# Performance work log

Hardware: AMD Instinct MI355X
Metric: run time of the kernel (lower is better)

## Reference

```python
import jax, jax.numpy as jnp
import numpy as np

DIM = 64
N = 10000
E = 40000


def setup_inputs() -> dict:
    key = jax.random.key(0)
    ks = jax.random.split(key, 16)
    def rn(k, shape, s):
        return jax.random.normal(k, shape, dtype=jnp.float32) * s
    inp = {}
    inp["x"] = jax.random.normal(ks[0], (N, 3), dtype=jnp.float32)
    inp["edge_attr"] = jax.random.uniform(ks[1], (E, 7), dtype=jnp.float32)
    inp["edge_index"] = jax.random.randint(ks[2], (2, E), 0, N)
    inp["batch"] = jnp.zeros((N,), dtype=jnp.int32)
    # lin0: Linear(3, dim)
    inp["lin0_w"] = rn(ks[3], (DIM, 3), 0.3)
    inp["lin0_b"] = jnp.zeros((DIM,), jnp.float32)
    # edge MLP: Linear(7, dim) -> ReLU -> Linear(dim, dim*dim)
    inp["em1_w"] = rn(ks[4], (DIM, 7), 0.3)
    inp["em1_b"] = jnp.zeros((DIM,), jnp.float32)
    inp["em2_w"] = rn(ks[5], (DIM * DIM, DIM), 0.05)
    inp["em2_b"] = jnp.zeros((DIM * DIM,), jnp.float32)
    # NNConv root weight [in, out] and bias
    inp["root_w"] = rn(ks[6], (DIM, DIM), 0.1)
    inp["conv_b"] = jnp.zeros((DIM,), jnp.float32)
    # GRU(dim, dim), gate order r, z, n
    inp["gru_wih"] = rn(ks[7], (3 * DIM, DIM), 0.1)
    inp["gru_whh"] = rn(ks[8], (3 * DIM, DIM), 0.1)
    inp["gru_bih"] = jnp.zeros((3 * DIM,), jnp.float32)
    inp["gru_bhh"] = jnp.zeros((3 * DIM,), jnp.float32)
    # Set2Set LSTM(2*dim, dim), gate order i, f, g, o
    inp["lstm_wih"] = rn(ks[9], (4 * DIM, 2 * DIM), 0.1)
    inp["lstm_whh"] = rn(ks[10], (4 * DIM, DIM), 0.1)
    inp["lstm_bih"] = jnp.zeros((4 * DIM,), jnp.float32)
    inp["lstm_bhh"] = jnp.zeros((4 * DIM,), jnp.float32)
    inp["lin1_w"] = rn(ks[11], (DIM, 2 * DIM), 0.1)
    inp["lin1_b"] = jnp.zeros((DIM,), jnp.float32)
    inp["lin3_w"] = rn(ks[12], (1, DIM), 0.1)
    inp["lin3_b"] = jnp.zeros((1,), jnp.float32)
    return inp


def _forward(x, edge_attr, lin0_w, lin0_b, em1_w, em1_b, em2_w, em2_b,
             root_w, conv_b, gru_wih, gru_whh, gru_bih, gru_bhh,
             lstm_wih, lstm_whh, lstm_bih, lstm_bhh,
             lin1_w, lin1_b, lin3_w, lin3_b, edge_index, batch):
    n = x.shape[0]
    dim = lin0_w.shape[0]
    src, dst = edge_index[0], edge_index[1]

    out = jax.nn.relu(x @ lin0_w.T + lin0_b)  # [N, dim]
    h = out                                   # GRU hidden state

    # Edge-conditioned weights depend only on edge_attr -> compute once.
    we = jax.nn.relu(edge_attr @ em1_w.T + em1_b) @ em2_w.T + em2_b
    we = we.reshape(-1, dim, dim)             # [E, dim, dim]

    deg = jax.ops.segment_sum(jnp.ones_like(src, dtype=x.dtype), dst, num_segments=n)
    inv_deg = jnp.where(deg > 0, 1.0 / jnp.maximum(deg, 1.0), 0.0)[:, None]

    for _ in range(6):
        # NNConv: per-edge matmul, scatter-mean, plus root transform
        msg = jnp.einsum('ei,eio->eo', out[src], we)            # [E, dim]
        agg = jax.ops.segment_sum(msg, dst, num_segments=n) * inv_deg
        m = jax.nn.relu(out @ root_w + agg + conv_b)            # [N, dim]
        # single-step GRU over nodes (seq_len=1, batch=N)
        gi = m @ gru_wih.T + gru_bih
        gh = h @ gru_whh.T + gru_bhh
        ir, iz, inew = jnp.split(gi, 3, axis=-1)
        hr, hz, hnew = jnp.split(gh, 3, axis=-1)
        r = jax.nn.sigmoid(ir + hr)
        z = jax.nn.sigmoid(iz + hz)
        ncand = jnp.tanh(inew + r * hnew)
        h = (1.0 - z) * ncand + z * h
        out = h

    # Set2Set pooling; single graph (batch is all zeros, pool.view(1,-1))
    q_star = jnp.zeros((1, 2 * dim), x.dtype)
    hl = jnp.zeros((1, dim), x.dtype)
    cl = jnp.zeros((1, dim), x.dtype)
    for _ in range(6):
        g = q_star @ lstm_wih.T + lstm_bih + hl @ lstm_whh.T + lstm_bhh
        gi_, gf_, gg_, go_ = jnp.split(g, 4, axis=-1)
        cl = jax.nn.sigmoid(gf_) * cl + jax.nn.sigmoid(gi_) * jnp.tanh(gg_)
        hl = jax.nn.sigmoid(go_) * jnp.tanh(cl)
        q = hl                                                  # [1, dim]
        e = jnp.einsum('nd,d->n', out, q[0])                    # attention logits
        a = jax.nn.softmax(e)                                   # softmax over the single graph
        r = jnp.einsum('n,nd->d', a, out)[None, :]              # readout [1, dim]
        q_star = jnp.concatenate([q, r], axis=-1)               # [1, 2*dim]

    pool = q_star.reshape(1, -1)
    hid = jax.nn.relu(pool @ lin1_w.T + lin1_b)
    return hid @ lin3_w.T + lin3_b                              # [1, 1]


def reference(x, edge_attr, edge_index, batch, lin0_w, lin0_b, em1_w, em1_b,
              em2_w, em2_b, root_w, conv_b, gru_wih, gru_whh, gru_bih, gru_bhh,
              lstm_wih, lstm_whh, lstm_bih, lstm_bhh, lin1_w, lin1_b, lin3_w, lin3_b):
    return _forward(x, edge_attr, lin0_w, lin0_b, em1_w, em1_b, em2_w, em2_b,
                    root_w, conv_b, gru_wih, gru_whh, gru_bih, gru_bhh,
                    lstm_wih, lstm_whh, lstm_bih, lstm_bhh,
                    lin1_w, lin1_b, lin3_w, lin3_b, edge_index, batch)
```

## Files before the change

### kernel.cpp

```cpp
#include <hip/hip_runtime.h>
#include <math.h>

#define NNODES 10000
#define NEDGES 40000
#define DIM 64
#define WS 200
#define EB 128
#define H1S 68
#define OTS 72
#define BSS 72

typedef short bf16x8 __attribute__((ext_vector_type(8)));
typedef float floatx4 __attribute__((ext_vector_type(4)));

__device__ __forceinline__ float sigmoidf_(float x) { return 1.0f / (1.0f + expf(-x)); }

__device__ __forceinline__ unsigned short f2bf(float x) {
    unsigned int u = __float_as_uint(x);
    u += 0x7fffu + ((u >> 16) & 1u);
    return (unsigned short)(u >> 16);
}
__device__ __forceinline__ float bf2f(unsigned short h) {
    return __uint_as_float(((unsigned int)h) << 16);
}
__device__ __forceinline__ unsigned int cvtpk(float lo, float hi) {
    unsigned int r;
    asm("v_cvt_pk_bf16_f32 %0, %1, %2" : "=v"(r) : "v"(lo), "v"(hi));
    return r;
}
__device__ __forceinline__ void write_split(unsigned short* __restrict__ p, int d, float v) {
    unsigned short hi = f2bf(v);
    unsigned short lo = f2bf(v - bf2f(hi));
    p[d] = hi;
    p[64 + d] = hi;
    p[128 + d] = lo;
}

__global__ __launch_bounds__(256) void k_prep(const float* __restrict__ x,
                                              const float* __restrict__ lin0_w,
                                              const float* __restrict__ lin0_b,
                                              float* __restrict__ out,
                                              unsigned short* __restrict__ Abf,
                                              const float* __restrict__ em2_w,
                                              const float* __restrict__ em2_b,
                                              unsigned short* __restrict__ Bek,
                                              const float* __restrict__ root_w,
                                              const float* __restrict__ gwih,
                                              const float* __restrict__ gwhh,
                                              unsigned short* __restrict__ Wcat,
                                              const float* __restrict__ lwih,
                                              const float* __restrict__ lwhh,
                                              float* __restrict__ wcT,
                                              float* __restrict__ wrT,
                                              const int* __restrict__ ei,
                                              int* __restrict__ counts,
                                              float* __restrict__ deg) {
    const int b = blockIdx.x;
    const int tid = threadIdx.x;
    if (b < 2500) {
        int idx = b * 256 + tid;
        if (idx >= NNODES * 64) return;
        int n = idx >> 6, d = idx & 63;
        float a = lin0_b[d];
        a += x[n * 3 + 0] * lin0_w[d * 3 + 0];
        a += x[n * 3 + 1] * lin0_w[d * 3 + 1];
        a += x[n * 3 + 2] * lin0_w[d * 3 + 2];
        float v = fmaxf(a, 0.0f);
        out[idx] = v;
        write_split(Abf + (size_t)n * 192, d, v);
    } else if (b < 3540) {
        int idx = (b - 2500) * 256 + tid;
        if (idx >= 4160 * 64) return;
        int r = idx >> 6, k = idx & 63;
        float v = (r < 4096) ? em2_w[(size_t)r * 64 + k] : em2_b[k * 64 + (r - 4096)];
        Bek[idx] = f2bf(v);
    } else if (b < 3652) {
        int idx = (b - 3540) * 256 + tid;
        if (idx >= 448 * 64) return;
        int r = idx >> 6, i = idx & 63;
        float v;
        if (r < 64) v = root_w[i * 64 + r];
        else if (r < 256) v = gwih[(r - 64) * 64 + i];
        else v = gwhh[(r - 256) * 64 + i];
        unsigned short hi = f2bf(v);
        unsigned short lo = f2bf(v - bf2f(hi));
        unsigned short* row = Wcat + (size_t)r * 192;
        row[i] = hi;
        row[64 + i] = lo;
        row[128 + i] = hi;
    } else if (b < 3780) {
        int idx = (b - 3652) * 256 + tid;
        if (idx < 64 * 256) {
            int k = idx >> 8, t = idx & 255;
            wcT[idx] = lwih[t * 128 + k] + lwhh[t * 64 + k];
        } else if (idx < 2 * 64 * 256) {
            int i2 = idx - 64 * 256;
            int k = i2 >> 8, t = i2 & 255;
            wrT[i2] = lwih[t * 128 + 64 + k];
        }
    } else {
        int e = (b - 3780) * 256 + tid;
        if (e < NEDGES) {
            atomicAdd(&counts[ei[e]], 1);
            atomicAdd(&deg[ei[NEDGES + e]], 1.0f);
        }
    }
}

__global__ __launch_bounds__(256) void k_scan(const int* __restrict__ counts,
                                              const float* __restrict__ deg,
                                              int* __restrict__ row_start,
                                              int* __restrict__ cursor,
                                              float* __restrict__ invd) {
    __shared__ int partial[256];
    const int tid = threadIdx.x;
    const int base = tid * 40;
    int local[40];
    int sum = 0;
#pragma unroll
    for (int i = 0; i < 40; ++i) {
        int idx = base + i;
        int v = (idx < NNODES) ? counts[idx] : 0;
        local[i] = sum;
        sum += v;
    }
    partial[tid] = sum;
    __syncthreads();
    for (int off = 1; off < 256; off <<= 1) {
        int t = (tid >= off) ? partial[tid - off] : 0;
        __syncthreads();
        partial[tid] += t;
        __syncthreads();
    }
    const int prev = (tid > 0) ? partial[tid - 1] : 0;
#pragma unroll
    for (int i = 0; i < 40; ++i) {
        int idx = base + i;
        if (idx < NNODES) {
            int rs = prev + local[i];
            row_start[idx] = rs;
            cursor[idx] = rs;
            float dg = deg[idx];
            invd[idx] = dg > 0.0f ? 1.0f / dg : 0.0f;
        }
    }
    if (tid == 255) row_start[NNODES] = partial[255];
}

__global__ __launch_bounds__(256) void k_edge(const int* __restrict__ ei,
                                              const float* __restrict__ ea,
                                              const float* __restrict__ w,
                                              const float* __restrict__ bvec,
                                              int* __restrict__ cursor,
                                              int* __restrict__ src_s,
                                              int* __restrict__ dst_s,
                                              float* __restrict__ h1s) {
    const int wv = threadIdx.x >> 6, lane = threadIdx.x & 63;
    const int e = blockIdx.x * 4 + wv;
    if (e >= NEDGES) return;
    int pos = 0;
    if (lane == 0) {
        int s = ei[e];
        pos = atomicAdd(&cursor[s], 1);
        src_s[pos] = s;
        dst_s[pos] = ei[NEDGES + e];
    }
    pos = __shfl(pos, 0);
    float a = bvec[lane];
#pragma unroll
    for (int j = 0; j < 7; ++j) a += ea[e * 7 + j] * w[lane * 7 + j];
    h1s[(size_t)pos * 64 + lane] = fmaxf(a, 0.0f);
}

__global__ __launch_bounds__(512) void k_econv(const float* __restrict__ out,
                                               const float* __restrict__ h1s,
                                               const unsigned short* __restrict__ Bek,
                                               const int* __restrict__ src_s,
                                               const int* __restrict__ dst_s,
                                               float* __restrict__ agg) {
    __shared__ __align__(16) float h1f[EB * H1S];
    __shared__ __align__(16) unsigned short out_t[EB * OTS];
    __shared__ __align__(16) unsigned short Bs[2][64 * BSS];
    const int tid = threadIdx.x;
    const int w = tid >> 6, lane = tid & 63;
    const int mi = lane & 15, q = lane >> 4;
    const int e0 = blockIdx.x * EB;
#pragma unroll
    for (int j = 0; j < 4; ++j) {
        int idx = tid + 512 * j;
        int r = idx >> 4, c4 = (idx & 15) * 4;
        int e = e0 + r;
        float4 h = make_float4(0.0f, 0.0f, 0.0f, 0.0f);
        float4 o4 = make_float4(0.0f, 0.0f, 0.0f, 0.0f);
        if (e < NEDGES) {
            h = *reinterpret_cast<const float4*>(&h1s[(size_t)e * 64 + c4]);
            int s = src_s[e];
            o4 = *reinterpret_cast<const float4*>(&out[(size_t)s * 64 + c4]);
        }
        *reinterpret_cast<float4*>(&h1f[r * H1S + c4]) = h;
        unsigned int p0 = (unsigned int)f2bf(o4.x) | ((unsigned int)f2bf(o4.y) << 16);
        unsigned int p1 = (unsigned int)f2bf(o4.z) | ((unsigned int)f2bf(o4.w) << 16);
        *reinterpret_cast<uint2*>(&out_t[r * OTS + c4]) = make_uint2(p0, p1);
    }
    {
        int r = tid >> 3, c8 = (tid & 7) * 8;
        *reinterpret_cast<uint4*>(&Bs[0][r * BSS + c8]) =
            *reinterpret_cast<const uint4*>(&Bek[(size_t)r * 64 + c8]);
    }
    __syncthreads();
    const int m = w * 16 + mi;
    float hreg[16];
#pragma unroll
    for (int j = 0; j < 8; ++j) {
        hreg[j]     = h1f[m * H1S + q * 8 + j];
        hreg[8 + j] = h1f[m * H1S + 32 + q * 8 + j];
    }
    floatx4 acc[4];
#pragma unroll
    for (int nt = 0; nt < 4; ++nt)
#pragma unroll
        for (int r = 0; r < 4; ++r) acc[nt][r] = 0.0f;
    int buf = 0;
    for (int c = 0; c <= 64; ++c) {
        if (c < 64) {
            int r = tid >> 3, c8 = (tid & 7) * 8;
            *reinterpret_cast<uint4*>(&Bs[buf ^ 1][r * BSS + c8]) =
                *reinterpret_cast<const uint4*>(&Bek[(size_t)(c + 1) * 4096 + r * 64 + c8]);
        }
        bf16x8 a0, a1;
        if (c < 64) {
            const float s = bf2f(out_t[m * OTS + c]);
            union { bf16x8 v; unsigned int u[4]; } A0, A1;
#pragma unroll
            for (int j = 0; j < 4; ++j) {
                A0.u[j] = cvtpk(s * hreg[2 * j],     s * hreg[2 * j + 1]);
                A1.u[j] = cvtpk(s * hreg[8 + 2 * j], s * hreg[8 + 2 * j + 1]);
            }
            a0 = A0.v;
            a1 = A1.v;
        } else {
            a0 = *reinterpret_cast<const bf16x8*>(&out_t[m * OTS + q * 8]);
            a1 = *reinterpret_cast<const bf16x8*>(&out_t[m * OTS + 32 + q * 8]);
        }
#pragma unroll
        for (int nt = 0; nt < 4; ++nt) {
            bf16x8 b0 = *reinterpret_cast<const bf16x8*>(&Bs[buf][(nt * 16 + mi) * BSS + q * 8]);
            bf16x8 b1 = *reinterpret_cast<const bf16x8*>(&Bs[buf][(nt * 16 + mi) * BSS + 32 + q * 8]);
            acc[nt] = __builtin_amdgcn_mfma_f32_16x16x32_bf16(a0, b0, acc[nt], 0, 0, 0);
            acc[nt] = __builtin_amdgcn_mfma_f32_16x16x32_bf16(a1, b1, acc[nt], 0, 0, 0);
        }
        __syncthreads();
        buf ^= 1;
    }
#pragma unroll
    for (int nt = 0; nt < 4; ++nt)
#pragma unroll
        for (int r = 0; r < 4; ++r)
            h1f[(w * 16 + q * 4 + r) * H1S + nt * 16 + mi] = acc[nt][r];
    __syncthreads();
#pragma unroll
    for (int rr = 0; rr < 16; ++rr) {
        int row = w * 16 + rr;
        int e = e0 + row;
        if (e < NEDGES)
            atomicAdd(&agg[(size_t)dst_s[e] * 64 + lane], h1f[row * H1S + lane]);
    }
}

__global__ __launch_bounds__(256) void k_node(float* __restrict__ agg,
                                              const float* __restrict__ invdeg,
                                              const unsigned short* __restrict__ Wcat,
                                              const float* __restrict__ conv_b,
                                              const float* __restrict__ bih,
                                              const float* __restrict__ bhh,
                                              float* __restrict__ out,
                                              unsigned short* __restrict__ Abf) {
    __shared__ unsigned short As[32 * WS];
    __shared__ unsigned short Ms[32 * WS];
    __shared__ float ho[32 * 68];
    const int tid = threadIdx.x;
    const int row0 = blockIdx.x * 32;
#pragma unroll
    for (int j = 0; j < 3; ++j) {
        int idx = tid + 256 * j;
        int r = idx / 24, jj = idx % 24;
        int ra = row0 + r; if (ra >= NNODES) ra = NNODES - 1;
        *reinterpret_cast<uint4*>(&As[r * WS + jj * 8]) =
            *reinterpret_cast<const uint4*>(&Abf[(size_t)ra * 192 + jj * 8]);
    }
#pragma unroll
    for (int j = 0; j < 2; ++j) {
        int idx = tid + 256 * j;
        int r = idx >> 4, c4 = (idx & 15) * 4;
        int ra = row0 + r; if (ra >= NNODES) ra = NNODES - 1;
        *reinterpret_cast<float4*>(&ho[r * 68 + c4]) =
            *reinterpret_cast<const float4*>(&out[(size_t)ra * 64 + c4]);
    }
    __syncthreads();
    const int wave = tid >> 6, lane = tid & 63;
    const int mi = lane & 15, q = lane >> 4;
    const int d = wave * 16 + mi;
    floatx4 gh[2][3];
#pragma unroll
    for (int rt = 0; rt < 2; ++rt)
#pragma unroll
        for (int g = 0; g < 3; ++g)
#pragma unroll
            for (int r = 0; r < 4; ++r) gh[rt][g][r] = 0.0f;
#pragma unroll
    for (int ks = 0; ks < 6; ++ks) {
        bf16x8 b[3];
#pragma unroll
        for (int g = 0; g < 3; ++g)
            b[g] = *reinterpret_cast<const bf16x8*>(&Wcat[(size_t)(256 + g * 64 + d) * 192 + ks * 32 + q * 8]);
#pragma unroll
        for (int rt = 0; rt < 2; ++rt) {
            bf16x8 a = *reinterpret_cast<const bf16x8*>(&As[(rt * 16 + mi) * WS + ks * 32 + q * 8]);
#pragma unroll
            for (int g = 0; g < 3; ++g)
                gh[rt][g] = __builtin_amdgcn_mfma_f32_16x16x32_bf16(a, b[g], gh[rt][g], 0, 0, 0);
        }
    }
    {
        floatx4 cm[2];
#pragma unroll
        for (int rt = 0; rt < 2; ++rt)
#pragma unroll
            for (int r = 0; r < 4; ++r) cm[rt][r] = 0.0f;
#pragma unroll
        for (int ks = 0; ks < 6; ++ks) {
            bf16x8 b = *reinterpret_cast<const bf16x8*>(&Wcat[(size_t)d * 192 + ks * 32 + q * 8]);
#pragma unroll
            for (int rt = 0; rt < 2; ++rt) {
                bf16x8 a = *reinterpret_cast<const bf16x8*>(&As[(rt * 16 + mi) * WS + ks * 32 + q * 8]);
                cm[rt] = __builtin_amdgcn_mfma_f32_16x16x32_bf16(a, b, cm[rt], 0, 0, 0);
            }
        }
        const float cb = conv_b[d];
#pragma unroll
        for (int rt = 0; rt < 2; ++rt) {
#pragma unroll
            for (int r = 0; r < 4; ++r) {
                int row = rt * 16 + q * 4 + r;
                int ra = row0 + row; int rc = (ra < NNODES) ? ra : NNODES - 1;
                float v = cm[rt][r] + agg[(size_t)rc * 64 + d] * invdeg[rc] + cb;
                if (ra < NNODES) agg[(size_t)ra * 64 + d] = 0.0f;
                v = fmaxf(v, 0.0f);
                unsigned short hi = f2bf(v);
                unsigned short lo = f2bf(v - bf2f(hi));
                Ms[row * WS + d] = hi;
                Ms[row * WS + 64 + d] = hi;
                Ms[row * WS + 128 + d] = lo;
            }
        }
    }
    __syncthreads();
    floatx4 gi[2][3];
#pragma unroll
    for (int rt = 0; rt < 2; ++rt)
#pragma unroll
        for (int g = 0; g < 3; ++g)
#pragma unroll
            for (int r = 0; r < 4; ++r) gi[rt][g][r] = 0.0f;
#pragma unroll
    for (int ks = 0; ks < 6; ++ks) {
        bf16x8 b[3];
#pragma unroll
        for (int g = 0; g < 3; ++g)
            b[g] = *reinterpret_cast<const bf16x8*>(&Wcat[(size_t)(64 + g * 64 + d) * 192 + ks * 32 + q * 8]);
#pragma unroll
        for (int rt = 0; rt < 2; ++rt) {
            bf16x8 a = *reinterpret_cast<const bf16x8*>(&Ms[(rt * 16 + mi) * WS + ks * 32 + q * 8]);
#pragma unroll
            for (int g = 0; g < 3; ++g)
                gi[rt][g] = __builtin_amdgcn_mfma_f32_16x16x32_bf16(a, b[g], gi[rt][g], 0, 0, 0);
        }
    }
    const float bi_r = bih[d], bi_z = bih[64 + d], bi_n = bih[128 + d];
    const float bh_r = bhh[d], bh_z = bhh[64 + d], bh_n = bhh[128 + d];
#pragma unroll
    for (int rt = 0; rt < 2; ++rt) {
#pragma unroll
        for (int r = 0; r < 4; ++r) {
            int row = rt * 16 + q * 4 + r;
            int ra = row0 + row;
            float rr = sigmoidf_(gi[rt][0][r] + bi_r + gh[rt][0][r] + bh_r);
            float zz = sigmoidf_(gi[rt][1][r] + bi_z + gh[rt][1][r] + bh_z);
            float nc = tanhf(gi[rt][2][r] + bi_n + rr * (gh[rt][2][r] + bh_n));
            float hn = (1.0f - zz) * nc + zz * ho[row * 68 + d];
            if (ra < NNODES) {
                out[(size_t)ra * 64 + d] = hn;
                write_split(Abf + (size_t)ra * 192, d, hn);
            }
        }
    }
}

__global__ __launch_bounds__(256) void k_step(const float* __restrict__ out,
                                              const float* __restrict__ wcT,
                                              const float* __restrict__ wrT,
                                              const float* __restrict__ bih,
                                              const float* __restrict__ bhh,
                                              float* __restrict__ hc,
                                              float* rs,
                                              int it) {
    __shared__ float outs[256 * 65];
    __shared__ float hl_s[64];
    __shared__ float qr[64];
    __shared__ float gsh[256];
    __shared__ float wsh[256];
    __shared__ float red[256];
    const int tid = threadIdx.x;
    const int n0 = blockIdx.x * 256;
#pragma unroll
    for (int j = 0; j < 16; ++j) {
        int idx = tid + 256 * j;
        int r = idx >> 4, c4 = (idx & 15) * 4;
        int n = n0 + r;
        float4 v = make_float4(0.0f, 0.0f, 0.0f, 0.0f);
        if (n < NNODES) v = *reinterpret_cast<const float4*>(&out[(size_t)n * 64 + c4]);
        outs[r * 65 + c4 + 0] = v.x;
        outs[r * 65 + c4 + 1] = v.y;
        outs[r * 65 + c4 + 2] = v.z;
        outs[r * 65 + c4 + 3] = v.w;
    }
    if (tid < 64) {
        hl_s[tid] = hc[it * 128 + tid];
        qr[tid] = (it > 0) ? rs[it * 68 + tid] / rs[it * 68 + 64] : 0.0f;
    }
    __syncthreads();
    float g0 = 0.0f, g1 = 0.0f, g2 = 0.0f, g3 = 0.0f;
#pragma unroll 4
    for (int k = 0; k < 64; k += 4) {
        g0 += hl_s[k + 0] * wcT[(k + 0) * 256 + tid] + qr[k + 0] * wrT[(k + 0) * 256 + tid];
        g1 += hl_s[k + 1] * wcT[(k + 1) * 256 + tid] + qr[k + 1] * wrT[(k + 1) * 256 + tid];
        g2 += hl_s[k + 2] * wcT[(k + 2) * 256 + tid] + qr[k + 2] * wrT[(k + 2) * 256 + tid];
        g3 += hl_s[k + 3] * wcT[(k + 3) * 256 + tid] + qr[k + 3] * wrT[(k + 3) * 256 + tid];
    }
    gsh[tid] = bih[tid] + bhh[tid] + ((g0 + g1) + (g2 + g3));
    __syncthreads();
    if (tid < 64) {
        float ig = sigmoidf_(gsh[tid]);
        float fg = sigmoidf_(gsh[64 + tid]);
        float gg = tanhf(gsh[128 + tid]);
        float og = sigmoidf_(gsh[192 + tid]);
        float c = fg * hc[it * 128 + 64 + tid] + ig * gg;
        float h = og * tanhf(c);
        hl_s[tid] = h;
        hc[(it + 1) * 128 + tid] = h;
        hc[(it + 1) * 128 + 64 + tid] = c;
    }
    __syncthreads();
    float w = 0.0f;
    if (n0 + tid < NNODES) {
        const float* row = &outs[tid * 65];
        float e0 = 0.0f, e1 = 0.0f, e2 = 0.0f, e3 = 0.0f;
#pragma unroll 8
        for (int k = 0; k < 64; k += 4) {
            e0 += row[k + 0] * hl_s[k + 0];
            e1 += row[k + 1] * hl_s[k + 1];
            e2 += row[k + 2] * hl_s[k + 2];
            e3 += row[k + 3] * hl_s[k + 3];
        }
        w = expf((e0 + e1) + (e2 + e3));
    }
    wsh[tid] = w;
    red[tid] = w;
    __syncthreads();
    for (int s = 128; s > 0; s >>= 1) {
        if (tid < s) red[tid] += red[tid + s];
        __syncthreads();
    }
    if (tid == 0) atomicAdd(&rs[(it + 1) * 68 + 64], red[0]);
    const int grp = tid >> 6, d = tid & 63;
    float a0 = 0.0f, a1 = 0.0f;
#pragma unroll 8
    for (int j = 0; j < 64; j += 2) {
        a0 += wsh[grp * 64 + j] * outs[(grp * 64 + j) * 65 + d];
        a1 += wsh[grp * 64 + j + 1] * outs[(grp * 64 + j + 1) * 65 + d];
    }
    atomicAdd(&rs[(it + 1) * 68 + d], a0 + a1);
}

__global__ __launch_bounds__(128) void k_out(const float* __restrict__ hc,
                                             const float* __restrict__ rs,
                                             const float* __restrict__ lin1_w,
                                             const float* __restrict__ lin1_b,
                                             const float* __restrict__ lin3_w,
                                             const float* __restrict__ lin3_b,
                                             float* __restrict__ dout) {
    __shared__ float qs[128];
    __shared__ float hs[64];
    int tid = threadIdx.x;
    qs[tid] = (tid < 64) ? hc[6 * 128 + tid] : rs[6 * 68 + (tid - 64)] / rs[6 * 68 + 64];
    __syncthreads();
    if (tid < 64) {
        float a = lin1_b[tid];
        for (int k = 0; k < 128; ++k) a += qs[k] * lin1_w[tid * 128 + k];
        hs[tid] = fmaxf(a, 0.0f);
    }
    __syncthreads();
    if (tid == 0) {
        float a = lin3_b[0];
        for (int k = 0; k < 64; ++k) a += hs[k] * lin3_w[k];
        dout[0] = a;
    }
}

extern "C" void kernel_launch(void* const* d_in, const int* in_sizes, int n_in,
                              void* d_out, int out_size, void* d_ws, size_t ws_size,
                              hipStream_t stream) {
    const float* x         = (const float*)d_in[0];
    const float* edge_attr = (const float*)d_in[1];
    const int*   ei        = (const int*)d_in[2];
    const float* lin0_w    = (const float*)d_in[4];
    const float* lin0_b    = (const float*)d_in[5];
    const float* em1_w     = (const float*)d_in[6];
    const float* em1_b     = (const float*)d_in[7];
    const float* em2_w     = (const float*)d_in[8];
    const float* em2_b     = (const float*)d_in[9];
    const float* root_w    = (const float*)d_in[10];
    const float* conv_b    = (const float*)d_in[11];
    const float* gru_wih   = (const float*)d_in[12];
    const float* gru_whh   = (const float*)d_in[13];
    const float* gru_bih   = (const float*)d_in[14];
    const float* gru_bhh   = (const float*)d_in[15];
    const float* lstm_wih  = (const float*)d_in[16];
    const float* lstm_whh  = (const float*)d_in[17];
    const float* lstm_bih  = (const float*)d_in[18];
    const float* lstm_bhh  = (const float*)d_in[19];
    const float* lin1_w    = (const float*)d_in[20];
    const float* lin1_b    = (const float*)d_in[21];
    const float* lin3_w    = (const float*)d_in[22];
    const float* lin3_b    = (const float*)d_in[23];

    float* ws = (float*)d_ws;
    size_t off = 0;
    unsigned short* Abf  = (unsigned short*)(ws + off); off += (size_t)NNODES * 192 / 2;
    unsigned short* Bek  = (unsigned short*)(ws + off); off += (size_t)4160 * 64 / 2;
    unsigned short* Wcat = (unsigned short*)(ws + off); off += (size_t)448 * 192 / 2;
    float* h1s   = ws + off; off += (size_t)NEDGES * 64;
    float* outb  = ws + off; off += (size_t)NNODES * 64;
    float* agg   = ws + off; off += (size_t)NNODES * 64;
    float* deg   = ws + off; off += NNODES;
    int*   counts    = (int*)(ws + off); off += NNODES;
    int*   cursor    = (int*)(ws + off); off += NNODES;
    int*   row_start = (int*)(ws + off); off += NNODES + 4;
    int*   src_s     = (int*)(ws + off); off += NEDGES;
    int*   dst_s     = (int*)(ws + off); off += NEDGES;
    float* invd  = ws + off; off += NNODES;
    float* wcT   = ws + off; off += 64 * 256;
    float* wrT   = ws + off; off += 64 * 256;
    float* rs    = ws + off; off += 7 * 68;
    float* hc    = ws + off; off += 7 * 128;

    hipMemsetAsync(deg, 0, 3 * NNODES * sizeof(float), stream);
    hipMemsetAsync(agg, 0, (size_t)NNODES * 64 * sizeof(float), stream);
    hipMemsetAsync(rs, 0, (7 * 68 + 7 * 128) * sizeof(float), stream);
    k_prep<<<3937, 256, 0, stream>>>(x, lin0_w, lin0_b, outb, Abf,
                                     em2_w, em2_b, Bek,
                                     root_w, gru_wih, gru_whh, Wcat,
                                     lstm_wih, lstm_whh, wcT, wrT,
                                     ei, counts, deg);
    k_scan<<<1, 256, 0, stream>>>(counts, deg, row_start, cursor, invd);
    k_edge<<<10000, 256, 0, stream>>>(ei, edge_attr, em1_w, em1_b, cursor, src_s, dst_s, h1s);

    const int neb = (NEDGES + EB - 1) / EB;
    for (int t = 0; t < 6; ++t) {
        k_econv<<<neb, 512, 0, stream>>>(outb, h1s, Bek, src_s, dst_s, agg);
        k_node<<<313, 256, 0, stream>>>(agg, invd, Wcat, conv_b, gru_bih, gru_bhh,
                                        outb, Abf);
    }

    for (int it = 0; it < 6; ++it)
        k_step<<<40, 256, 0, stream>>>(outb, wcT, wrT, lstm_bih, lstm_bhh, hc, rs, it);
    k_out<<<1, 128, 0, stream>>>(hc, rs, lin1_w, lin1_b, lin3_w, lin3_b, (float*)d_out);
}
```

Measured before the change: 661.2 us.

## Shrink edge-conv blocks, stage two B chunks per barrier, atomics from registers

Edge tile size drops from 128 to 64 edges with 256 threads, which doubles the block count and cuts shared memory per block. The per-edge hidden vectors now load straight from global into registers instead of through an LDS staging buffer. The B weight chunks are staged two at a time into a 4-slot buffer, which halves the number of barriers in the 65-chunk loop. The scatter-add to agg is issued directly from MFMA accumulator registers rather than through an LDS transpose. The direct atomics hit scattered addresses with less coalescing, and the bounds checks are dropped because 40000 divides evenly by 64.

```diff
diff --git a/kernel.cpp b/kernel.cpp
--- a/kernel.cpp
+++ b/kernel.cpp
@@ -5,8 +5,7 @@
 #define NEDGES 40000
 #define DIM 64
 #define WS 200
-#define EB 128
-#define H1S 68
+#define EB 64
 #define OTS 72
 #define BSS 72
 
@@ -172,61 +171,54 @@
     h1s[(size_t)pos * 64 + lane] = fmaxf(a, 0.0f);
 }
 
-__global__ __launch_bounds__(512) void k_econv(const float* __restrict__ out,
+__global__ __launch_bounds__(256) void k_econv(const float* __restrict__ out,
                                                const float* __restrict__ h1s,
                                                const unsigned short* __restrict__ Bek,
                                                const int* __restrict__ src_s,
                                                const int* __restrict__ dst_s,
                                                float* __restrict__ agg) {
-    __shared__ __align__(16) float h1f[EB * H1S];
+    __shared__ __align__(16) unsigned short Bs[4][64 * BSS];
     __shared__ __align__(16) unsigned short out_t[EB * OTS];
-    __shared__ __align__(16) unsigned short Bs[2][64 * BSS];
     const int tid = threadIdx.x;
     const int w = tid >> 6, lane = tid & 63;
     const int mi = lane & 15, q = lane >> 4;
     const int e0 = blockIdx.x * EB;
 #pragma unroll
     for (int j = 0; j < 4; ++j) {
-        int idx = tid + 512 * j;
+        int idx = tid + 256 * j;
         int r = idx >> 4, c4 = (idx & 15) * 4;
-        int e = e0 + r;
-        float4 h = make_float4(0.0f, 0.0f, 0.0f, 0.0f);
-        float4 o4 = make_float4(0.0f, 0.0f, 0.0f, 0.0f);
-        if (e < NEDGES) {
-            h = *reinterpret_cast<const float4*>(&h1s[(size_t)e * 64 + c4]);
-            int s = src_s[e];
-            o4 = *reinterpret_cast<const float4*>(&out[(size_t)s * 64 + c4]);
-        }
-        *reinterpret_cast<float4*>(&h1f[r * H1S + c4]) = h;
+        int s = src_s[e0 + r];
+        float4 o4 = *reinterpret_cast<const float4*>(&out[(size_t)s * 64 + c4]);
         unsigned int p0 = (unsigned int)f2bf(o4.x) | ((unsigned int)f2bf(o4.y) << 16);
         unsigned int p1 = (unsigned int)f2bf(o4.z) | ((unsigned int)f2bf(o4.w) << 16);
         *reinterpret_cast<uint2*>(&out_t[r * OTS + c4]) = make_uint2(p0, p1);
     }
-    {
-        int r = tid >> 3, c8 = (tid & 7) * 8;
-        *reinterpret_cast<uint4*>(&Bs[0][r * BSS + c8]) =
-            *reinterpret_cast<const uint4*>(&Bek[(size_t)r * 64 + c8]);
-    }
-    __syncthreads();
     const int m = w * 16 + mi;
     float hreg[16];
-#pragma unroll
-    for (int j = 0; j < 8; ++j) {
-        hreg[j]     = h1f[m * H1S + q * 8 + j];
-        hreg[8 + j] = h1f[m * H1S + 32 + q * 8 + j];
-    }
+    {
+        const float4* hp = reinterpret_cast<const float4*>(&h1s[(size_t)(e0 + m) * 64]);
+        float4 h0 = hp[q * 2], h1v = hp[q * 2 + 1];
+        float4 h2 = hp[8 + q * 2], h3 = hp[8 + q * 2 + 1];
+        hreg[0] = h0.x; hreg[1] = h0.y; hreg[2] = h0.z; hreg[3] = h0.w;
+        hreg[4] = h1v.x; hreg[5] = h1v.y; hreg[6] = h1v.z; hreg[7] = h1v.w;
+        hreg[8] = h2.x; hreg[9] = h2.y; hreg[10] = h2.z; hreg[11] = h2.w;
+        hreg[12] = h3.x; hreg[13] = h3.y; hreg[14] = h3.z; hreg[15] = h3.w;
+    }
+    auto stageB = [&](int chunk, unsigned short* dst) {
+#pragma unroll
+        for (int j = 0; j < 2; ++j) {
+            int idx = tid + 256 * j;
+            int r = idx >> 3, c8 = (idx & 7) * 8;
+            *reinterpret_cast<uint4*>(&dst[r * BSS + c8]) =
+                *reinterpret_cast<const uint4*>(&Bek[(size_t)chunk * 4096 + r * 64 + c8]);
+        }
+    };
     floatx4 acc[4];
 #pragma unroll
     for (int nt = 0; nt < 4; ++nt)
 #pragma unroll
         for (int r = 0; r < 4; ++r) acc[nt][r] = 0.0f;
-    int buf = 0;
-    for (int c = 0; c <= 64; ++c) {
-        if (c < 64) {
-            int r = tid >> 3, c8 = (tid & 7) * 8;
-            *reinterpret_cast<uint4*>(&Bs[buf ^ 1][r * BSS + c8]) =
-                *reinterpret_cast<const uint4*>(&Bek[(size_t)(c + 1) * 4096 + r * 64 + c8]);
-        }
+    auto computeC = [&](int c, const unsigned short* bsp) {
         bf16x8 a0, a1;
         if (c < 64) {
             const float s = bf2f(out_t[m * OTS + c]);
@@ -244,27 +236,42 @@
         }
 #pragma unroll
         for (int nt = 0; nt < 4; ++nt) {
-            bf16x8 b0 = *reinterpret_cast<const bf16x8*>(&Bs[buf][(nt * 16 + mi) * BSS + q * 8]);
-            bf16x8 b1 = *reinterpret_cast<const bf16x8*>(&Bs[buf][(nt * 16 + mi) * BSS + 32 + q * 8]);
+            bf16x8 b0 = *reinterpret_cast<const bf16x8*>(&bsp[(nt * 16 + mi) * BSS + q * 8]);
+            bf16x8 b1 = *reinterpret_cast<const bf16x8*>(&bsp[(nt * 16 + mi) * BSS + 32 + q * 8]);
             acc[nt] = __builtin_amdgcn_mfma_f32_16x16x32_bf16(a0, b0, acc[nt], 0, 0, 0);
             acc[nt] = __builtin_amdgcn_mfma_f32_16x16x32_bf16(a1, b1, acc[nt], 0, 0, 0);
         }
+    };
+    stageB(0, Bs[0]);
+    stageB(1, Bs[1]);
+    __syncthreads();
+    for (int p = 0; p < 33; ++p) {
+        if (p < 32) {
+            const int nb = ((p + 1) & 1) * 2;
+            if (p + 1 < 32) {
+                stageB(2 * (p + 1), Bs[nb]);
+                stageB(2 * (p + 1) + 1, Bs[nb + 1]);
+            } else {
+                stageB(64, Bs[nb]);
+            }
+        }
+        const int cb = (p & 1) * 2;
+        if (p < 32) {
+            computeC(2 * p, Bs[cb]);
+            computeC(2 * p + 1, Bs[cb + 1]);
+        } else {
+            computeC(64, Bs[cb]);
+        }
         __syncthreads();
-        buf ^= 1;
-    }
+    }
+    int dd[4];
+#pragma unroll
+    for (int r = 0; r < 4; ++r) dd[r] = dst_s[e0 + w * 16 + q * 4 + r];
 #pragma unroll
     for (int nt = 0; nt < 4; ++nt)
 #pragma unroll
         for (int r = 0; r < 4; ++r)
-            h1f[(w * 16 + q * 4 + r) * H1S + nt * 16 + mi] = acc[nt][r];
-    __syncthreads();
-#pragma unroll
-    for (int rr = 0; rr < 16; ++rr) {
-        int row = w * 16 + rr;
-        int e = e0 + row;
-        if (e < NEDGES)
-            atomicAdd(&agg[(size_t)dst_s[e] * 64 + lane], h1f[row * H1S + lane]);
-    }
+            atomicAdd(&agg[(size_t)dd[r] * 64 + nt * 16 + mi], acc[nt][r]);
 }
 
 __global__ __launch_bounds__(256) void k_node(float* __restrict__ agg,
@@ -565,9 +572,9 @@
     k_scan<<<1, 256, 0, stream>>>(counts, deg, row_start, cursor, invd);
     k_edge<<<10000, 256, 0, stream>>>(ei, edge_attr, em1_w, em1_b, cursor, src_s, dst_s, h1s);
 
-    const int neb = (NEDGES + EB - 1) / EB;
+    const int neb = NEDGES / EB;
     for (int t = 0; t < 6; ++t) {
-        k_econv<<<neb, 512, 0, stream>>>(outb, h1s, Bek, src_s, dst_s, agg);
+        k_econv<<<neb, 256, 0, stream>>>(outb, h1s, Bek, src_s, dst_s, agg);
         k_node<<<313, 256, 0, stream>>>(agg, invd, Wcat, conv_b, gru_bih, gru_bhh,
                                         outb, Abf);
     }
```

Result: faster. 594.9 us (-10.0%).
